# Kernel optimization log

Measured on AMD Instinct MI355X. Metric: run time of the kernel, lower is better.

## Reference

```python
import jax, jax.numpy as jnp
import numpy as np
import math

B, S, E, H, FF = 2, 2048, 768, 12, 3072
D = E // H
SCALING = 1.0
EPS = 1e-5


def layer_norm(x, g, b):
    mu = jnp.mean(x, axis=-1, keepdims=True)
    var = jnp.var(x, axis=-1, keepdims=True)
    return (x - mu) * jax.lax.rsqrt(var + EPS) * g + b


def setup_inputs() -> dict:
    key = jax.random.key(0)
    ks = jax.random.split(key, 16)
    s_e = 1.0 / math.sqrt(E)
    s_f = 1.0 / math.sqrt(FF)
    inp = {
        "x": jax.random.normal(ks[0], (B, S, E), dtype=jnp.float32),
        "Wq": jax.random.uniform(ks[1], (E, E), jnp.float32, -s_e, s_e),
        "bq": jnp.zeros((E,), jnp.float32),
        "Wk": jax.random.uniform(ks[2], (E, E), jnp.float32, -s_e, s_e),
        "bk": jnp.zeros((E,), jnp.float32),
        "Wv": jax.random.uniform(ks[3], (E, E), jnp.float32, -s_e, s_e),
        "bv": jnp.zeros((E,), jnp.float32),
        "Wo": jax.random.uniform(ks[4], (E, E), jnp.float32, -s_e, s_e),
        "bo": jnp.zeros((E,), jnp.float32),
        "W1": jax.random.uniform(ks[5], (E, FF), jnp.float32, -s_e, s_e),
        "b1": jnp.zeros((FF,), jnp.float32),
        "W2": jax.random.uniform(ks[6], (FF, E), jnp.float32, -s_f, s_f),
        "b2": jnp.zeros((E,), jnp.float32),
        "g1": jnp.ones((E,), jnp.float32),
        "be1": jnp.zeros((E,), jnp.float32),
        "g2": jnp.ones((E,), jnp.float32),
        "be2": jnp.zeros((E,), jnp.float32),
    }
    return inp


def reference(x, Wq, bq, Wk, bk, Wv, bv, Wo, bo, W1, b1, W2, b2, g1, be1, g2, be2):
    # --- multi-head attention with ALiBi-style symmetric distance bias ---
    q = (x @ Wq + bq).reshape(B, S, H, D)
    k = (x @ Wk + bk).reshape(B, S, H, D)
    v = (x @ Wv + bv).reshape(B, S, H, D)
    scores = jnp.einsum("bqhd,bkhd->bhqk", q, k) / math.sqrt(D)
    pos = jnp.arange(S)
    alibi = -SCALING * jnp.abs(pos[None, :] - pos[:, None]).astype(jnp.float32)  # [S,S]
    scores = scores + alibi  # broadcast over [B,H]
    attn_map = jax.nn.softmax(scores, axis=-1)  # [B,H,S,S]
    ctx = jnp.einsum("bhqk,bkhd->bqhd", attn_map, v).reshape(B, S, E)
    attn_out = ctx @ Wo + bo
    # --- residual + norm, FFN, residual + norm (dropout = eval/identity) ---
    h = layer_norm(x + attn_out, g1, be1)
    ff = jax.nn.relu(h @ W1 + b1) @ W2 + b2
    out = layer_norm(h + ff, g2, be2)
    return (out, attn_map)
```

## Files before the change

### kernel.cpp

```cpp
#include <hip/hip_runtime.h>
#include <stdint.h>

static constexpr int cB = 2, cS = 2048, cE = 768, cH = 12, cFF = 3072, cD = 64;
static constexpr int cM = cB * cS;

typedef __bf16 bf16x8 __attribute__((ext_vector_type(8)));
typedef float f32x4 __attribute__((ext_vector_type(4)));

__device__ __forceinline__ unsigned short f2bf(float f) {
    union { float f; unsigned int u; } v; v.f = f;
    unsigned int r = v.u + 0x7fffu + ((v.u >> 16) & 1u);
    return (unsigned short)(r >> 16);
}

__device__ __forceinline__ void load_lds16(const unsigned short* g, unsigned short* l) {
    __builtin_amdgcn_global_load_lds(
        (const __attribute__((address_space(1))) unsigned int*)(g),
        (__attribute__((address_space(3))) unsigned int*)(l), 16, 0, 0);
}

template<int BM, int BN, int EPI>
__global__ __launch_bounds__(256, 4) void gemm_nt(
    const unsigned short* __restrict__ Ab,
    const unsigned short* __restrict__ Btp,
    float* __restrict__ outF,
    unsigned short* __restrict__ outB,
    unsigned short* __restrict__ outB2,
    const float* __restrict__ bias0,
    const float* __restrict__ bias1,
    const float* __restrict__ bias2,
    const float* __restrict__ resid,
    int M, int N, int K, long sB)
{
    constexpr int MI = BM / 32, NI = BN / 32;
    __shared__ alignas(16) unsigned short Sh[BM * 64 + BN * 64];
    unsigned short* Al = Sh;
    unsigned short* Bl = Sh + BM * 64;
    const int tid = threadIdx.x;
    const int lane = tid & 63, wave = tid >> 6;
    const int wm = wave >> 1, wn = wave & 1;
    const int bz = blockIdx.z;
    const int m0 = blockIdx.y * BM, n0 = blockIdx.x * BN;
    const int ln = lane & 15, lg = lane >> 4;
    const int sw = ln & 7;

    const unsigned short* Bt = Btp + (size_t)bz * sB;

    f32x4 acc[MI][NI];
#pragma unroll
    for (int i = 0; i < MI; i++)
#pragma unroll
        for (int j = 0; j < NI; j++) acc[i][j] = (f32x4){0.f, 0.f, 0.f, 0.f};

    for (int k0 = 0; k0 < K; k0 += 64) {
        __syncthreads();
#pragma unroll
        for (int it = 0; it < BM / 32; ++it) {
            int idx = tid + it * 256;
            int r = idx >> 3, c8 = idx & 7;
            int cs = c8 ^ (r & 7);
            load_lds16(Ab + (size_t)(m0 + r) * K + k0 + cs * 8, &Al[idx * 8]);
        }
#pragma unroll
        for (int it = 0; it < BN / 32; ++it) {
            int idx = tid + it * 256;
            int r = idx >> 3, c8 = idx & 7;
            int cs = c8 ^ (r & 7);
            load_lds16(Bt + (size_t)(n0 + r) * K + k0 + cs * 8, &Bl[idx * 8]);
        }
        __syncthreads();
#pragma unroll
        for (int ks = 0; ks < 2; ++ks) {
            bf16x8 av[MI], bv[NI];
#pragma unroll
            for (int i = 0; i < MI; i++) {
                int row = wm * (BM / 2) + 16 * i + ln;
                av[i] = *(const bf16x8*)&Al[row * 64 + ((ks * 4 + lg) ^ sw) * 8];
            }
#pragma unroll
            for (int j = 0; j < NI; j++) {
                int row = wn * (BN / 2) + 16 * j + ln;
                bv[j] = *(const bf16x8*)&Bl[row * 64 + ((ks * 4 + lg) ^ sw) * 8];
            }
#pragma unroll
            for (int i = 0; i < MI; i++)
#pragma unroll
                for (int j = 0; j < NI; j++)
                    acc[i][j] = __builtin_amdgcn_mfma_f32_16x16x32_bf16(av[i], bv[j], acc[i][j], 0, 0, 0);
        }
    }

    if constexpr (EPI == 0) {
        if (bz < 2) {
            const float* bia = (bz == 0) ? bias0 : bias1;
#pragma unroll
            for (int i = 0; i < MI; i++)
#pragma unroll
                for (int j = 0; j < NI; j++)
#pragma unroll
                    for (int r = 0; r < 4; r++) {
                        int m = m0 + wm * (BM / 2) + 16 * i + lg * 4 + r;
                        int n = n0 + wn * (BN / 2) + 16 * j + ln;
                        float v = acc[i][j][r] + bia[n];
                        int b = m >> 11, s = m & 2047, h = n >> 6, d = n & 63;
                        outB[(size_t)bz * ((size_t)cB * cH * cS * cD) +
                             ((((size_t)b * cH + h) * cS + s) << 6) + d] = f2bf(v);
                    }
        } else {
            constexpr int TS = BM + 8;
            __syncthreads();
#pragma unroll
            for (int i = 0; i < MI; i++)
#pragma unroll
                for (int j = 0; j < NI; j++)
#pragma unroll
                    for (int r = 0; r < 4; r++) {
                        int ml = wm * (BM / 2) + 16 * i + lg * 4 + r;
                        int nl = wn * (BN / 2) + 16 * j + ln;
                        Sh[nl * TS + ml] = f2bf(acc[i][j][r] + bias2[n0 + nl]);
                    }
            __syncthreads();
            const int b = m0 >> 11, sbase = m0 & 2047;
#pragma unroll
            for (int it = 0; it < (BN * BM / 8) / 256; ++it) {
                int idx = tid + it * 256;
                int rr = idx >> 4, c8 = idx & 15;
                uint4 val = *(const uint4*)&Sh[rr * TS + c8 * 8];
                int ng = n0 + rr;
                int h = ng >> 6, d = ng & 63;
                *(uint4*)&outB2[((((size_t)b * cH + h) << 6) + d) * (size_t)cS + sbase + c8 * 8] = val;
            }
        }
    } else {
#pragma unroll
        for (int i = 0; i < MI; i++) {
#pragma unroll
            for (int j = 0; j < NI; j++) {
#pragma unroll
                for (int r = 0; r < 4; r++) {
                    int m = m0 + wm * (BM / 2) + 16 * i + lg * 4 + r;
                    int n = n0 + wn * (BN / 2) + 16 * j + ln;
                    float v = acc[i][j][r];
                    if constexpr (EPI == 3) {
                        v += bias0[n] + resid[(size_t)m * N + n];
                        outF[(size_t)m * N + n] = v;
                    } else {
                        v = fmaxf(v + bias0[n], 0.f);
                        outB[(size_t)m * N + n] = f2bf(v);
                    }
                }
            }
        }
    }
}

__global__ __launch_bounds__(256, 3) void attn_fused(
    const unsigned short* __restrict__ Qh,
    const unsigned short* __restrict__ Kh,
    const unsigned short* __restrict__ Vt,
    float* __restrict__ attn,
    unsigned short* __restrict__ ctxb)
{
    constexpr int VS = 136;
    __shared__ alignas(16) unsigned short Kl[128 * 64];
    __shared__ alignas(16) unsigned short Vl[64 * 128];
    __shared__ alignas(16) unsigned short Pb[64 * VS];
    __shared__ float rs2[2][64];
    __shared__ float rsinv[64];

    const int tid = threadIdx.x;
    const int lane = tid & 63, wave = tid >> 6;
    const int wm = wave >> 1, wn = wave & 1;
    const int ln = lane & 15, lg = lane >> 4;
    const int sw = ln & 7;
    const int m0 = blockIdx.x * 64;
    const int bh = blockIdx.y;

    const int nt_lo = max(0, (m0 - 120) / 128);
    const int nt_hi = min(15, (m0 + 183) / 128);

    const unsigned short* Qg = Qh + ((size_t)bh * cS + m0) * cD;
    const unsigned short* Kg = Kh + (size_t)bh * cS * cD;
    const unsigned short* Vg = Vt + (size_t)bh * cD * cS;
    float* attng = attn + (size_t)bh * cS * cS;

#pragma unroll
    for (int it = 0; it < 2; ++it) {
        int idx = tid + it * 256;
        int r = idx >> 3, c8 = idx & 7;
        int cs = c8 ^ (r & 7);
        load_lds16(Qg + r * cD + cs * 8, &Vl[idx * 8]);
    }
    __syncthreads();
    bf16x8 qf[2][2];
#pragma unroll
    for (int ks = 0; ks < 2; ++ks)
#pragma unroll
        for (int i = 0; i < 2; i++)
            qf[ks][i] = *(const bf16x8*)&Vl[(wm * 32 + 16 * i + ln) * 64 + ((ks * 4 + lg) ^ sw) * 8];

    float psum[8];
#pragma unroll
    for (int k = 0; k < 8; k++) psum[k] = 0.f;

    for (int nt = nt_lo; nt <= nt_hi; ++nt) {
        __syncthreads();
#pragma unroll
        for (int it = 0; it < 4; ++it) {
            int idx = tid + it * 256;
            int r = idx >> 3, c8 = idx & 7;
            int cs = c8 ^ (r & 7);
            load_lds16(Kg + (size_t)(nt * 128 + r) * cD + cs * 8, &Kl[idx * 8]);
        }
        __syncthreads();
        f32x4 acc[2][4];
#pragma unroll
        for (int i = 0; i < 2; i++)
#pragma unroll
            for (int j = 0; j < 4; j++) acc[i][j] = (f32x4){0.f, 0.f, 0.f, 0.f};
#pragma unroll
        for (int ks = 0; ks < 2; ++ks) {
            bf16x8 b[4];
#pragma unroll
            for (int j = 0; j < 4; j++)
                b[j] = *(const bf16x8*)&Kl[(wn * 64 + 16 * j + ln) * 64 + ((ks * 4 + lg) ^ sw) * 8];
#pragma unroll
            for (int i = 0; i < 2; i++)
#pragma unroll
                for (int j = 0; j < 4; j++)
                    acc[i][j] = __builtin_amdgcn_mfma_f32_16x16x32_bf16(qf[ks][i], b[j], acc[i][j], 0, 0, 0);
        }
#pragma unroll
        for (int i = 0; i < 2; i++)
#pragma unroll
            for (int j = 0; j < 4; j++)
#pragma unroll
                for (int r = 0; r < 4; r++) {
                    int mg = m0 + wm * 32 + 16 * i + lg * 4 + r;
                    int ng = nt * 128 + wn * 64 + 16 * j + ln;
                    psum[i * 4 + r] += __expf(acc[i][j][r] * 0.125f - fabsf((float)(mg - ng)));
                }
    }
#pragma unroll
    for (int k = 0; k < 8; k++) {
        float v = psum[k];
        v += __shfl_xor(v, 1); v += __shfl_xor(v, 2);
        v += __shfl_xor(v, 4); v += __shfl_xor(v, 8);
        psum[k] = v;
    }
    if (ln == 0) {
#pragma unroll
        for (int i = 0; i < 2; i++)
#pragma unroll
            for (int r = 0; r < 4; r++)
                rs2[wn][wm * 32 + 16 * i + lg * 4 + r] = psum[i * 4 + r];
    }
    __syncthreads();
    if (tid < 64) rsinv[tid] = 1.f / (rs2[0][tid] + rs2[1][tid]);
    __syncthreads();
    float invl[8];
#pragma unroll
    for (int i = 0; i < 2; i++)
#pragma unroll
        for (int r = 0; r < 4; r++)
            invl[i * 4 + r] = rsinv[wm * 32 + 16 * i + lg * 4 + r];

    f32x4 oacc[2][2];
#pragma unroll
    for (int i = 0; i < 2; i++)
#pragma unroll
        for (int j = 0; j < 2; j++) oacc[i][j] = (f32x4){0.f, 0.f, 0.f, 0.f};

    for (int nt = nt_lo; nt <= nt_hi; ++nt) {
        __syncthreads();
#pragma unroll
        for (int it = 0; it < 4; ++it) {
            int idx = tid + it * 256;
            int r = idx >> 3, c8 = idx & 7;
            int cs = c8 ^ (r & 7);
            load_lds16(Kg + (size_t)(nt * 128 + r) * cD + cs * 8, &Kl[idx * 8]);
        }
#pragma unroll
        for (int it = 0; it < 4; ++it) {
            int idx = tid + it * 256;
            int r = idx >> 4, c8 = idx & 15;
            int cs = c8 ^ (r & 7);
            load_lds16(Vg + (size_t)r * cS + nt * 128 + cs * 8, &Vl[idx * 8]);
        }
        __syncthreads();
        f32x4 acc[2][4];
#pragma unroll
        for (int i = 0; i < 2; i++)
#pragma unroll
            for (int j = 0; j < 4; j++) acc[i][j] = (f32x4){0.f, 0.f, 0.f, 0.f};
#pragma unroll
        for (int ks = 0; ks < 2; ++ks) {
            bf16x8 b[4];
#pragma unroll
            for (int j = 0; j < 4; j++)
                b[j] = *(const bf16x8*)&Kl[(wn * 64 + 16 * j + ln) * 64 + ((ks * 4 + lg) ^ sw) * 8];
#pragma unroll
            for (int i = 0; i < 2; i++)
#pragma unroll
                for (int j = 0; j < 4; j++)
                    acc[i][j] = __builtin_amdgcn_mfma_f32_16x16x32_bf16(qf[ks][i], b[j], acc[i][j], 0, 0, 0);
        }
#pragma unroll
        for (int i = 0; i < 2; i++)
#pragma unroll
            for (int j = 0; j < 4; j++)
#pragma unroll
                for (int r = 0; r < 4; r++) {
                    int mloc = wm * 32 + 16 * i + lg * 4 + r;
                    int nloc = wn * 64 + 16 * j + ln;
                    int mg = m0 + mloc, ng = nt * 128 + nloc;
                    float p = __expf(acc[i][j][r] * 0.125f - fabsf((float)(mg - ng))) * invl[i * 4 + r];
                    attng[(size_t)mg * cS + ng] = p;
                    Pb[mloc * VS + nloc] = f2bf(p);
                }
        __syncthreads();
#pragma unroll
        for (int ks = 0; ks < 4; ++ks) {
            bf16x8 pa[2], vb[2];
#pragma unroll
            for (int i = 0; i < 2; i++)
                pa[i] = *(const bf16x8*)&Pb[(wm * 32 + 16 * i + ln) * VS + ks * 32 + lg * 8];
#pragma unroll
            for (int j = 0; j < 2; j++) {
                int row = wn * 32 + 16 * j + ln;
                vb[j] = *(const bf16x8*)&Vl[row * 128 + ((ks * 4 + lg) ^ sw) * 8];
            }
#pragma unroll
            for (int i = 0; i < 2; i++)
#pragma unroll
                for (int j = 0; j < 2; j++)
                    oacc[i][j] = __builtin_amdgcn_mfma_f32_16x16x32_bf16(pa[i], vb[j], oacc[i][j], 0, 0, 0);
        }
    }
    {
        int b = bh / cH, h = bh % cH;
#pragma unroll
        for (int i = 0; i < 2; i++)
#pragma unroll
            for (int j = 0; j < 2; j++)
#pragma unroll
                for (int r = 0; r < 4; r++) {
                    int mg = m0 + wm * 32 + 16 * i + lg * 4 + r;
                    int d = wn * 32 + 16 * j + ln;
                    ctxb[((size_t)b * cS + mg) * cE + h * 64 + d] = f2bf(oacc[i][j][r]);
                }
    }
    {
        const f32x4 z4 = {0.f, 0.f, 0.f, 0.f};
        const int c4lo = nt_lo * 32;
        const int c4hi = (nt_hi + 1) * 32;
        for (int r = wave; r < 64; r += 4) {
            f32x4* rowp = (f32x4*)(attng + (size_t)(m0 + r) * cS);
            for (int c = lane; c < c4lo; c += 64) rowp[c] = z4;
            for (int c = c4hi + lane; c < 512; c += 64) rowp[c] = z4;
        }
    }
}

template<bool WH>
__global__ __launch_bounds__(256) void layernorm_k(const float* __restrict__ in,
    const float* __restrict__ g, const float* __restrict__ be,
    float* __restrict__ outF, unsigned short* __restrict__ outB)
{
    const size_t row = blockIdx.x;
    const float* p = in + row * cE;
    const int tid = threadIdx.x;
    float x0 = p[tid], x1 = p[tid + 256], x2 = p[tid + 512];
    float sum = x0 + x1 + x2, sq = x0 * x0 + x1 * x1 + x2 * x2;
    __shared__ float s1[4], s2[4];
    for (int o = 32; o; o >>= 1) { sum += __shfl_xor(sum, o); sq += __shfl_xor(sq, o); }
    if ((tid & 63) == 0) { s1[tid >> 6] = sum; s2[tid >> 6] = sq; }
    __syncthreads();
    sum = s1[0] + s1[1] + s1[2] + s1[3];
    sq  = s2[0] + s2[1] + s2[2] + s2[3];
    float mu = sum * (1.f / cE);
    float var = sq * (1.f / cE) - mu * mu;
    float rstd = rsqrtf(var + 1e-5f);
#pragma unroll
    for (int i = 0; i < 3; i++) {
        int c = tid + 256 * i;
        float xv = (i == 0) ? x0 : ((i == 1) ? x1 : x2);
        float y = (xv - mu) * rstd * g[c] + be[c];
        outF[row * cE + c] = y;
        if constexpr (WH) outB[row * cE + c] = f2bf(y);
    }
}

__global__ __launch_bounds__(256) void prep_all(
    const float* __restrict__ x, unsigned short* __restrict__ xb,
    const float* __restrict__ Wq, const float* __restrict__ Wk,
    const float* __restrict__ Wv, const float* __restrict__ Wo,
    const float* __restrict__ W1, const float* __restrict__ W2,
    unsigned short* __restrict__ Wqt, unsigned short* __restrict__ W1t,
    unsigned short* __restrict__ W2t)
{
    __shared__ float t[32][33];
    int bid = blockIdx.x;
    if (bid < 3072) {
        int i = bid * 256 + threadIdx.x;
        float4 v = ((const float4*)x)[i];
        ushort4 o;
        o.x = f2bf(v.x); o.y = f2bf(v.y); o.z = f2bf(v.z); o.w = f2bf(v.w);
        ((ushort4*)xb)[i] = o;
        return;
    }
    bid -= 3072;
    const float* src; unsigned short* dst; int R, C, tx, ty;
    if (bid < 2304) {
        int m = bid / 576, tt = bid - m * 576;
        src = (m == 0) ? Wq : (m == 1) ? Wk : (m == 2) ? Wv : Wo;
        dst = Wqt + (size_t)m * 589824;
        R = 768; C = 768; tx = tt % 24; ty = tt / 24;
    } else if (bid < 4608) {
        int tt = bid - 2304;
        src = W1; dst = W1t; R = 768; C = 3072; tx = tt % 96; ty = tt / 96;
    } else {
        int tt = bid - 4608;
        src = W2; dst = W2t; R = 3072; C = 768; tx = tt % 24; ty = tt / 24;
    }
    int c0 = tx * 32, r0 = ty * 32;
    int lx = threadIdx.x & 31, ly = threadIdx.x >> 5;
#pragma unroll
    for (int i = 0; i < 32; i += 8) t[ly + i][lx] = src[(size_t)(r0 + ly + i) * C + c0 + lx];
    __syncthreads();
#pragma unroll
    for (int i = 0; i < 32; i += 8) dst[(size_t)(c0 + ly + i) * R + r0 + lx] = f2bf(t[lx][ly + i]);
}

extern "C" void kernel_launch(void* const* d_in, const int* in_sizes, int n_in,
                              void* d_out, int out_size, void* d_ws, size_t ws_size,
                              hipStream_t stream)
{
    const float* x   = (const float*)d_in[0];
    const float* Wq  = (const float*)d_in[1];
    const float* bq  = (const float*)d_in[2];
    const float* Wk  = (const float*)d_in[3];
    const float* bk  = (const float*)d_in[4];
    const float* Wv  = (const float*)d_in[5];
    const float* bv  = (const float*)d_in[6];
    const float* Wo  = (const float*)d_in[7];
    const float* bo  = (const float*)d_in[8];
    const float* W1  = (const float*)d_in[9];
    const float* b1  = (const float*)d_in[10];
    const float* W2  = (const float*)d_in[11];
    const float* b2  = (const float*)d_in[12];
    const float* g1  = (const float*)d_in[13];
    const float* be1 = (const float*)d_in[14];
    const float* g2  = (const float*)d_in[15];
    const float* be2 = (const float*)d_in[16];

    float* out  = (float*)d_out;
    float* attn = out + (size_t)cB * cS * cE;

    char* ws = (char*)d_ws;
    unsigned short* xb   = (unsigned short*)(ws + 0);
    unsigned short* ctxb = xb;
    unsigned short* Wqt  = (unsigned short*)(ws + 6291456);
    unsigned short* W1t  = (unsigned short*)(ws + 11010048);
    unsigned short* W2t  = (unsigned short*)(ws + 15728640);
    unsigned short* Qh   = (unsigned short*)(ws + 20447232);
    unsigned short* Kh   = (unsigned short*)(ws + 26738688);
    unsigned short* Vt   = (unsigned short*)(ws + 33030144);
    unsigned short* ff1b = Qh;
    float* res1 = (float*)(ws + 45613056);
    float* res2 = res1;
    float* hf   = (float*)(ws + 58195968);
    unsigned short* hb = (unsigned short*)(ws + 70778880);

    prep_all<<<9984, 256, 0, stream>>>(x, xb, Wq, Wk, Wv, Wo, W1, W2, Wqt, W1t, W2t);
    gemm_nt<128, 96, 0><<<dim3(8, 32, 3), 256, 0, stream>>>(
        xb, Wqt, nullptr, Qh, Vt, bq, bk, bv, nullptr, cM, cE, cE, 589824);
    attn_fused<<<dim3(cS / 64, cB * cH), 256, 0, stream>>>(Qh, Kh, Vt, attn, ctxb);
    gemm_nt<128, 96, 3><<<dim3(8, 32, 1), 256, 0, stream>>>(
        ctxb, Wqt + 3 * 589824, res1, nullptr, nullptr, bo, nullptr, nullptr, x, cM, cE, cE, 0);
    layernorm_k<true><<<cM, 256, 0, stream>>>(res1, g1, be1, hf, hb);
    gemm_nt<128, 96, 4><<<dim3(32, 32, 1), 256, 0, stream>>>(
        hb, W1t, nullptr, ff1b, nullptr, b1, nullptr, nullptr, nullptr, cM, cFF, cE, 0);
    gemm_nt<128, 96, 3><<<dim3(8, 32, 1), 256, 0, stream>>>(
        ff1b, W2t, res2, nullptr, nullptr, b2, nullptr, nullptr, hf, cM, cE, cFF, 0);
    layernorm_k<false><<<cM, 256, 0, stream>>>(res2, g2, be2, out, nullptr);
}
```

Baseline: 630.8 us.

## Move attention-map zero fill into GEMM epilogues and split-K the E-output GEMMs

The far-off-band zeroing of the attention map moves out of the attention kernel. It is spread across the Wo, W1 and W2 GEMM blocks, each of which clears a fixed slice of attention rows with nontemporal stores, so that bandwidth-bound fill overlaps with compute-bound GEMMs. The two N=768 GEMMs (Wo and W2) now use split-K into two partial buffers, doubling their grid from 256 to 512 blocks for better CU occupancy. The layernorm kernels sum the two partials. The cost is extra partial-buffer traffic and workspace aliasing that must line up with the buffer lifetimes.

```diff
diff --git a/kernel.cpp b/kernel.cpp
--- a/kernel.cpp
+++ b/kernel.cpp
@@ -18,18 +18,22 @@
         (const __attribute__((address_space(1))) unsigned int*)(g),
         (__attribute__((address_space(3))) unsigned int*)(l), 16, 0, 0);
 }
+
+static constexpr int ZJOBS_PER_BLOCK = 12288;
 
 template<int BM, int BN, int EPI>
 __global__ __launch_bounds__(256, 4) void gemm_nt(
     const unsigned short* __restrict__ Ab,
     const unsigned short* __restrict__ Btp,
     float* __restrict__ outF,
+    float* __restrict__ outF2,
     unsigned short* __restrict__ outB,
     unsigned short* __restrict__ outB2,
     const float* __restrict__ bias0,
     const float* __restrict__ bias1,
     const float* __restrict__ bias2,
     const float* __restrict__ resid,
+    float* __restrict__ zattn, int zbase,
     int M, int N, int K, long sB)
 {
     constexpr int MI = BM / 32, NI = BN / 32;
@@ -52,7 +56,10 @@
 #pragma unroll
         for (int j = 0; j < NI; j++) acc[i][j] = (f32x4){0.f, 0.f, 0.f, 0.f};
 
-    for (int k0 = 0; k0 < K; k0 += 64) {
+    int kbeg = 0, kend = K;
+    if constexpr (EPI == 3) { int kh = K >> 1; kbeg = bz * kh; kend = kbeg + kh; }
+
+    for (int k0 = kbeg; k0 < kend; k0 += 64) {
         __syncthreads();
 #pragma unroll
         for (int it = 0; it < BM / 32; ++it) {
@@ -87,6 +94,26 @@
 #pragma unroll
                 for (int j = 0; j < NI; j++)
                     acc[i][j] = __builtin_amdgcn_mfma_f32_16x16x32_bf16(av[i], bv[j], acc[i][j], 0, 0, 0);
+        }
+    }
+
+    if constexpr (EPI == 3 || EPI == 4) {
+        const int lin = blockIdx.x + gridDim.x * (blockIdx.y + gridDim.y * blockIdx.z);
+        const size_t zb = (size_t)(zbase + lin) * ZJOBS_PER_BLOCK;
+        const f32x4 z4 = {0.f, 0.f, 0.f, 0.f};
+        f32x4* zp = (f32x4*)zattn;
+        for (int jj = tid; jj < ZJOBS_PER_BLOCK; jj += 256) {
+            size_t j = zb + jj;
+            int row  = (int)(j >> 9);
+            int slot = (int)(j & 511);
+            int m064 = (row & 2047) & ~63;
+            int ntlo = (m064 > 120) ? ((m064 - 120) >> 7) : 0;
+            int nthi = (m064 + 183) >> 7; nthi = nthi > 15 ? 15 : nthi;
+            int zlo = ntlo << 5;
+            int span = ((nthi + 1) << 5) - zlo;
+            int chunk = slot < zlo ? slot : slot + span;
+            if (chunk < 512)
+                __builtin_nontemporal_store(z4, zp + ((size_t)row << 9) + chunk);
         }
     }
 
@@ -131,7 +158,8 @@
                 *(uint4*)&outB2[((((size_t)b * cH + h) << 6) + d) * (size_t)cS + sbase + c8 * 8] = val;
             }
         }
-    } else {
+    } else if constexpr (EPI == 3) {
+        float* o = (bz == 0) ? outF : outF2;
 #pragma unroll
         for (int i = 0; i < MI; i++) {
 #pragma unroll
@@ -141,13 +169,22 @@
                     int m = m0 + wm * (BM / 2) + 16 * i + lg * 4 + r;
                     int n = n0 + wn * (BN / 2) + 16 * j + ln;
                     float v = acc[i][j][r];
-                    if constexpr (EPI == 3) {
-                        v += bias0[n] + resid[(size_t)m * N + n];
-                        outF[(size_t)m * N + n] = v;
-                    } else {
-                        v = fmaxf(v + bias0[n], 0.f);
-                        outB[(size_t)m * N + n] = f2bf(v);
-                    }
+                    if (bz == 0) v += bias0[n] + resid[(size_t)m * N + n];
+                    o[(size_t)m * N + n] = v;
+                }
+            }
+        }
+    } else {
+#pragma unroll
+        for (int i = 0; i < MI; i++) {
+#pragma unroll
+            for (int j = 0; j < NI; j++) {
+#pragma unroll
+                for (int r = 0; r < 4; r++) {
+                    int m = m0 + wm * (BM / 2) + 16 * i + lg * 4 + r;
+                    int n = n0 + wn * (BN / 2) + 16 * j + ln;
+                    float v = fmaxf(acc[i][j][r] + bias0[n], 0.f);
+                    outB[(size_t)m * N + n] = f2bf(v);
                 }
             }
         }
@@ -350,20 +387,11 @@
                     ctxb[((size_t)b * cS + mg) * cE + h * 64 + d] = f2bf(oacc[i][j][r]);
                 }
     }
-    {
-        const f32x4 z4 = {0.f, 0.f, 0.f, 0.f};
-        const int c4lo = nt_lo * 32;
-        const int c4hi = (nt_hi + 1) * 32;
-        for (int r = wave; r < 64; r += 4) {
-            f32x4* rowp = (f32x4*)(attng + (size_t)(m0 + r) * cS);
-            for (int c = lane; c < c4lo; c += 64) rowp[c] = z4;
-            for (int c = c4hi + lane; c < 512; c += 64) rowp[c] = z4;
-        }
-    }
-}
-
-template<bool WH>
+}
+
+template<bool WH, bool TWO>
 __global__ __launch_bounds__(256) void layernorm_k(const float* __restrict__ in,
+    const float* __restrict__ in2,
     const float* __restrict__ g, const float* __restrict__ be,
     float* __restrict__ outF, unsigned short* __restrict__ outB)
 {
@@ -371,6 +399,10 @@
     const float* p = in + row * cE;
     const int tid = threadIdx.x;
     float x0 = p[tid], x1 = p[tid + 256], x2 = p[tid + 512];
+    if constexpr (TWO) {
+        const float* q = in2 + row * cE;
+        x0 += q[tid]; x1 += q[tid + 256]; x2 += q[tid + 512];
+    }
     float sum = x0 + x1 + x2, sq = x0 * x0 + x1 * x1 + x2 * x2;
     __shared__ float s1[4], s2[4];
     for (int o = 32; o; o >>= 1) { sum += __shfl_xor(sum, o); sq += __shfl_xor(sq, o); }
@@ -467,21 +499,27 @@
     unsigned short* Kh   = (unsigned short*)(ws + 26738688);
     unsigned short* Vt   = (unsigned short*)(ws + 33030144);
     unsigned short* ff1b = Qh;
-    float* res1 = (float*)(ws + 45613056);
-    float* res2 = res1;
-    float* hf   = (float*)(ws + 58195968);
+    float* res1a = (float*)(ws + 45613056);
+    float* res1b = (float*)(ws + 58195968);
+    float* hf    = res1a;
+    float* res2a = (float*)(ws + 58195968);
+    float* res2b = (float*)(ws + 0);
     unsigned short* hb = (unsigned short*)(ws + 70778880);
 
     prep_all<<<9984, 256, 0, stream>>>(x, xb, Wq, Wk, Wv, Wo, W1, W2, Wqt, W1t, W2t);
     gemm_nt<128, 96, 0><<<dim3(8, 32, 3), 256, 0, stream>>>(
-        xb, Wqt, nullptr, Qh, Vt, bq, bk, bv, nullptr, cM, cE, cE, 589824);
+        xb, Wqt, nullptr, nullptr, Qh, Vt, bq, bk, bv, nullptr, nullptr, 0,
+        cM, cE, cE, 589824);
     attn_fused<<<dim3(cS / 64, cB * cH), 256, 0, stream>>>(Qh, Kh, Vt, attn, ctxb);
-    gemm_nt<128, 96, 3><<<dim3(8, 32, 1), 256, 0, stream>>>(
-        ctxb, Wqt + 3 * 589824, res1, nullptr, nullptr, bo, nullptr, nullptr, x, cM, cE, cE, 0);
-    layernorm_k<true><<<cM, 256, 0, stream>>>(res1, g1, be1, hf, hb);
+    gemm_nt<128, 96, 3><<<dim3(8, 32, 2), 256, 0, stream>>>(
+        ctxb, Wqt + 3 * 589824, res1a, res1b, nullptr, nullptr, bo, nullptr, nullptr, x,
+        attn, 0, cM, cE, cE, 0);
+    layernorm_k<true, true><<<cM, 256, 0, stream>>>(res1a, res1b, g1, be1, hf, hb);
     gemm_nt<128, 96, 4><<<dim3(32, 32, 1), 256, 0, stream>>>(
-        hb, W1t, nullptr, ff1b, nullptr, b1, nullptr, nullptr, nullptr, cM, cFF, cE, 0);
-    gemm_nt<128, 96, 3><<<dim3(8, 32, 1), 256, 0, stream>>>(
-        ff1b, W2t, res2, nullptr, nullptr, b2, nullptr, nullptr, hf, cM, cE, cFF, 0);
-    layernorm_k<false><<<cM, 256, 0, stream>>>(res2, g2, be2, out, nullptr);
-}
+        hb, W1t, nullptr, nullptr, ff1b, nullptr, b1, nullptr, nullptr, nullptr,
+        attn, 512, cM, cFF, cE, 0);
+    gemm_nt<128, 96, 3><<<dim3(8, 32, 2), 256, 0, stream>>>(
+        ff1b, W2t, res2a, res2b, nullptr, nullptr, b2, nullptr, nullptr, hf,
+        attn, 1536, cM, cE, cFF, 0);
+    layernorm_k<false, true><<<cM, 256, 0, stream>>>(res2a, res2b, g2, be2, out, nullptr);
+}
```

Measured after the change: 609.8 us. 3.3% less time.
